# Performance work log

Measured on AMD Instinct MI355X. Metric: run time of the kernel, lower is better.

## Reference

```python
import jax, jax.numpy as jnp
import numpy as np

IN_F = 2048
OUT_F = 2048
BATCH = 8192
ACT_BITS = 4
EPS = 1e-5


def setup_inputs() -> dict:
    key = jax.random.key(0)
    kx, kw, kb = jax.random.split(key, 3)
    x = jax.random.normal(kx, (BATCH, IN_F), dtype=jnp.float32)
    # kaiming-uniform-like init: bound = sqrt(6/fan_in) with a=sqrt(5) -> gain sqrt(2/(1+5))
    bound_w = float(np.sqrt(6.0 / (1.0 + 5.0)) / np.sqrt(IN_F))
    weight = jax.random.uniform(kw, (OUT_F, IN_F), minval=-bound_w, maxval=bound_w, dtype=jnp.float32)
    bound_b = float(1.0 / np.sqrt(IN_F))
    bias = jax.random.uniform(kb, (OUT_F,), minval=-bound_b, maxval=bound_b, dtype=jnp.float32)
    return {"x": x, "weight": weight, "bias": bias}


def _ste_sign(x):
    return x + jax.lax.stop_gradient(jnp.sign(x) - x)


def _ste_clip(x, lo, hi):
    return x + jax.lax.stop_gradient(jnp.clip(x, lo, hi) - x)


def reference(x, weight, bias):
    # weight binarization (ternary-ish via sign of mean-centered rows)
    w_centered = weight - jnp.mean(weight, axis=1, keepdims=True)
    w_bin = _ste_sign(w_centered)                       # [out, in]
    beta = jnp.mean(jnp.abs(weight), axis=1)[None, :]   # [1, out]
    # layer norm (no affine) over last dim
    mu = jnp.mean(x, axis=-1, keepdims=True)
    var = jnp.mean((x - mu) ** 2, axis=-1, keepdims=True)
    xln = (x - mu) / jnp.sqrt(var + EPS)
    qb = float(2 ** (ACT_BITS - 1) - 1)
    gama = jnp.maximum(jnp.max(jnp.abs(xln), axis=-1, keepdims=True), EPS)  # [B,1]
    xq = _ste_clip(xln * (qb / gama), -qb + EPS, qb - EPS)
    y = jnp.einsum('bi,oi->bo', xq, w_bin)
    y = y * (beta * gama / qb)
    return y + bias
```

## Files before the change

### kernel.cpp

```cpp
#include <hip/hip_runtime.h>
#include <hip/hip_bf16.h>

#define BATCH 8192
#define IN_F  2048
#define OUT_F 2048
#define QB    7.0f
#define EPSV  1e-5f
#define ASCALE 18.0f

typedef char  i8x4 __attribute__((ext_vector_type(4)));
typedef int   i32x4 __attribute__((ext_vector_type(4)));

#define AS1(p) ((__attribute__((address_space(1))) void*)(p))
#define AS3(p) ((__attribute__((address_space(3))) void*)(p))

__device__ __forceinline__ float waveReduceSum(float v) {
#pragma unroll
  for (int off = 32; off > 0; off >>= 1) v += __shfl_xor(v, off, 64);
  return v;
}
__device__ __forceinline__ float waveReduceMax(float v) {
#pragma unroll
  for (int off = 32; off > 0; off >>= 1) v = fmaxf(v, __shfl_xor(v, off, 64));
  return v;
}

__global__ __launch_bounds__(256) void prep_kernel(const float* __restrict__ x,
                                                   const float* __restrict__ w,
                                                   char* __restrict__ xq,
                                                   char* __restrict__ wb,
                                                   float* __restrict__ gamaOut,
                                                   float* __restrict__ betaOut) {
  __shared__ float red[8];
  const int t = threadIdx.x;
  const int wave = t >> 6, lane = t & 63;

  if (blockIdx.x < OUT_F) {
    const int row = blockIdx.x;
    const float* wr = w + (size_t)row * IN_F;
    float4 v0 = ((const float4*)wr)[t];
    float4 v1 = ((const float4*)wr)[t + 256];
    float s  = v0.x + v0.y + v0.z + v0.w + v1.x + v1.y + v1.z + v1.w;
    float sa = fabsf(v0.x) + fabsf(v0.y) + fabsf(v0.z) + fabsf(v0.w)
             + fabsf(v1.x) + fabsf(v1.y) + fabsf(v1.z) + fabsf(v1.w);
    float wsum = waveReduceSum(s);
    float wsa  = waveReduceSum(sa);
    if (lane == 0) { red[wave] = wsum; red[4 + wave] = wsa; }
    __syncthreads();
    const float mu   = (red[0] + red[1] + red[2] + red[3]) * (1.0f / IN_F);
    const float beta = (red[4] + red[5] + red[6] + red[7]) * (1.0f / IN_F);
    if (t == 0) betaOut[row] = beta;

    char* wbr = wb + (size_t)row * IN_F;
    auto sgn = [&](float xv) -> char {
      float d = xv - mu;
      return (char)((d > 0.0f) ? 1 : (d < 0.0f ? -1 : 0));
    };
    i8x4 q0 = { sgn(v0.x), sgn(v0.y), sgn(v0.z), sgn(v0.w) };
    i8x4 q1 = { sgn(v1.x), sgn(v1.y), sgn(v1.z), sgn(v1.w) };
    ((i8x4*)wbr)[t]       = q0;
    ((i8x4*)wbr)[t + 256] = q1;
  } else {
    const int row = blockIdx.x - OUT_F;
    const float* xr = x + (size_t)row * IN_F;
    float4 v0 = ((const float4*)xr)[t];
    float4 v1 = ((const float4*)xr)[t + 256];
    float s  = v0.x + v0.y + v0.z + v0.w + v1.x + v1.y + v1.z + v1.w;
    float s2 = v0.x*v0.x + v0.y*v0.y + v0.z*v0.z + v0.w*v0.w
             + v1.x*v1.x + v1.y*v1.y + v1.z*v1.z + v1.w*v1.w;
    float wsum  = waveReduceSum(s);
    float wsum2 = waveReduceSum(s2);
    if (lane == 0) { red[wave] = wsum; red[4 + wave] = wsum2; }
    __syncthreads();
    const float mu  = (red[0] + red[1] + red[2] + red[3]) * (1.0f / IN_F);
    const float ex2 = (red[4] + red[5] + red[6] + red[7]) * (1.0f / IN_F);
    const float rstd = rsqrtf(fmaxf(ex2 - mu * mu, 0.0f) + EPSV);

    float n[8];
    n[0] = (v0.x - mu) * rstd; n[1] = (v0.y - mu) * rstd;
    n[2] = (v0.z - mu) * rstd; n[3] = (v0.w - mu) * rstd;
    n[4] = (v1.x - mu) * rstd; n[5] = (v1.y - mu) * rstd;
    n[6] = (v1.z - mu) * rstd; n[7] = (v1.w - mu) * rstd;
    float amax = 0.0f;
#pragma unroll
    for (int j = 0; j < 8; ++j) amax = fmaxf(amax, fabsf(n[j]));

    __syncthreads();
    float wmax = waveReduceMax(amax);
    if (lane == 0) red[wave] = wmax;
    __syncthreads();
    const float g = fmaxf(fmaxf(fmaxf(red[0], red[1]), fmaxf(red[2], red[3])), EPSV);
    if (t == 0) gamaOut[row] = g;

    const float qs = (QB * ASCALE) / g;
    const float lo = (-QB + EPSV) * ASCALE, hi = (QB - EPSV) * ASCALE;
    auto qz = [&](float v) -> char {
      return (char)__float2int_rn(fminf(fmaxf(v * qs, lo), hi));
    };
    char* xqr = xq + (size_t)row * IN_F;
    i8x4 q0 = { qz(n[0]), qz(n[1]), qz(n[2]), qz(n[3]) };
    i8x4 q1 = { qz(n[4]), qz(n[5]), qz(n[6]), qz(n[7]) };
    ((i8x4*)xqr)[t]       = q0;
    ((i8x4*)xqr)[t + 256] = q1;
  }
}

__global__ __launch_bounds__(256) void gemm_kernel(const char* __restrict__ A,
                                                   const char* __restrict__ B,
                                                   const float* __restrict__ beta,
                                                   const float* __restrict__ gama,
                                                   const float* __restrict__ bias,
                                                   float* __restrict__ out) {
  __shared__ __align__(16) char As[128 * 128];
  __shared__ __align__(16) char Bs[128 * 128];

  const int t = threadIdx.x;
  const int wave = t >> 6, lane = t & 63;
  const int mBase = blockIdx.y * 128;
  const int nBase = blockIdx.x * 128;
  const int wm = (wave >> 1) * 64;
  const int wn = (wave & 1) * 64;

  i32x4 acc[4][4];
#pragma unroll
  for (int i = 0; i < 4; ++i)
#pragma unroll
    for (int j = 0; j < 4; ++j) {
      i32x4 z = {0, 0, 0, 0};
      acc[i][j] = z;
    }

  const int lr = lane >> 3;
  const int ls = lane & 7;
  const int gch = (ls - lr) & 7;
  const char* aG[4];
  const char* bG[4];
  char* aL[4];
  char* bL[4];
#pragma unroll
  for (int j = 0; j < 4; ++j) {
    const int rowInTile = j * 32 + wave * 8 + lr;
    aG[j] = A + (size_t)(mBase + rowInTile) * IN_F + gch * 16;
    bG[j] = B + (size_t)(nBase + rowInTile) * IN_F + gch * 16;
    aL[j] = As + (j * 32 + wave * 8) * 128;
    bL[j] = Bs + (j * 32 + wave * 8) * 128;
  }

  const int fr = lane & 15;
  const int kq = lane >> 4;
  const char* aF = As + (wm + fr) * 128;
  const char* bF = Bs + (wn + fr) * 128;
  int koff[2];
#pragma unroll
  for (int ks = 0; ks < 2; ++ks) koff[ks] = ((ks * 4 + kq + fr) & 7) * 16;

  for (int k0 = 0; k0 < IN_F; k0 += 128) {
#pragma unroll
    for (int j = 0; j < 4; ++j) {
      __builtin_amdgcn_global_load_lds(AS1(aG[j] + k0), AS3(aL[j]), 16, 0, 0);
      __builtin_amdgcn_global_load_lds(AS1(bG[j] + k0), AS3(bL[j]), 16, 0, 0);
    }
    __syncthreads();

#pragma unroll
    for (int ks = 0; ks < 2; ++ks) {
      i32x4 af[4], bf[4];
#pragma unroll
      for (int mi = 0; mi < 4; ++mi) af[mi] = *(const i32x4*)(aF + mi * 16 * 128 + koff[ks]);
#pragma unroll
      for (int ni = 0; ni < 4; ++ni) bf[ni] = *(const i32x4*)(bF + ni * 16 * 128 + koff[ks]);
#pragma unroll
      for (int mi = 0; mi < 4; ++mi)
#pragma unroll
        for (int ni = 0; ni < 4; ++ni)
          acc[mi][ni] = __builtin_amdgcn_mfma_i32_16x16x64_i8(af[mi], bf[ni], acc[mi][ni], 0, 0, 0);
    }
    __syncthreads();
  }

  const float qinv = 1.0f / (QB * ASCALE);
  const int orow0 = mBase + wm + (kq << 2);
  const int ocol0 = nBase + wn + fr;
#pragma unroll
  for (int mi = 0; mi < 4; ++mi) {
    const int rbase = orow0 + mi * 16;
    const float g0 = gama[rbase + 0] * qinv;
    const float g1 = gama[rbase + 1] * qinv;
    const float g2 = gama[rbase + 2] * qinv;
    const float g3 = gama[rbase + 3] * qinv;
#pragma unroll
    for (int ni = 0; ni < 4; ++ni) {
      const int c = ocol0 + ni * 16;
      const float bsc = beta[c];
      const float bv  = bias[c];
      float* op = out + (size_t)rbase * OUT_F + c;
      op[0 * OUT_F] = (float)acc[mi][ni][0] * (bsc * g0) + bv;
      op[1 * OUT_F] = (float)acc[mi][ni][1] * (bsc * g1) + bv;
      op[2 * OUT_F] = (float)acc[mi][ni][2] * (bsc * g2) + bv;
      op[3 * OUT_F] = (float)acc[mi][ni][3] * (bsc * g3) + bv;
    }
  }
}

extern "C" void kernel_launch(void* const* d_in, const int* in_sizes, int n_in,
                              void* d_out, int out_size, void* d_ws, size_t ws_size,
                              hipStream_t stream) {
  const float* x      = (const float*)d_in[0];
  const float* weight = (const float*)d_in[1];
  const float* bias   = (const float*)d_in[2];
  float* out = (float*)d_out;

  char* ws = (char*)d_ws;
  char* wbin = ws;
  char* xq   = ws + (size_t)OUT_F * IN_F;
  float* betaW = (float*)(ws + (size_t)OUT_F * IN_F + (size_t)BATCH * IN_F);
  float* gamaX = betaW + OUT_F;

  prep_kernel<<<OUT_F + BATCH, 256, 0, stream>>>(x, weight, xq, wbin, gamaX, betaW);
  gemm_kernel<<<dim3(OUT_F / 128, BATCH / 128), 256, 0, stream>>>(xq, wbin, betaW, gamaX, bias, out);
}
```

Before: 170.2 us.

## Double-buffer int8 GEMM LDS tiles with K=64 stages to overlap loads

Splits the shared-memory A/B tiles into two 64-wide K buffers and prefetches the next K slice with global_load_lds while MFMAs run on the current one. This cuts the barriers per iteration from two to one and aims to hide global-to-LDS latency. The swizzle is adapted to 4 chunks per row. Risks: twice as many loop iterations with less MFMA work each, and possible reliance on the single barrier to order the async LDS loads.

```diff
diff --git a/kernel.cpp b/kernel.cpp
--- a/kernel.cpp
+++ b/kernel.cpp
@@ -111,8 +111,8 @@
                                                    const float* __restrict__ gama,
                                                    const float* __restrict__ bias,
                                                    float* __restrict__ out) {
-  __shared__ __align__(16) char As[128 * 128];
-  __shared__ __align__(16) char Bs[128 * 128];
+  __shared__ __align__(16) char As[2][128 * 64];
+  __shared__ __align__(16) char Bs[2][128 * 64];
 
   const int t = threadIdx.x;
   const int wave = t >> 6, lane = t & 63;
@@ -130,52 +130,60 @@
       acc[i][j] = z;
     }
 
-  const int lr = lane >> 3;
-  const int ls = lane & 7;
-  const int gch = (ls - lr) & 7;
-  const char* aG[4];
-  const char* bG[4];
-  char* aL[4];
-  char* bL[4];
-#pragma unroll
-  for (int j = 0; j < 4; ++j) {
-    const int rowInTile = j * 32 + wave * 8 + lr;
+  const int lr = lane >> 2;
+  const int ls = lane & 3;
+  const int gch = (ls - (lr >> 1)) & 3;
+  const char* aG[2];
+  const char* bG[2];
+  int ldsOff[2];
+#pragma unroll
+  for (int j = 0; j < 2; ++j) {
+    const int rowInTile = wave * 32 + j * 16 + lr;
     aG[j] = A + (size_t)(mBase + rowInTile) * IN_F + gch * 16;
     bG[j] = B + (size_t)(nBase + rowInTile) * IN_F + gch * 16;
-    aL[j] = As + (j * 32 + wave * 8) * 128;
-    bL[j] = Bs + (j * 32 + wave * 8) * 128;
+    ldsOff[j] = (wave * 32 + j * 16) * 64;
   }
 
   const int fr = lane & 15;
   const int kq = lane >> 4;
-  const char* aF = As + (wm + fr) * 128;
-  const char* bF = Bs + (wn + fr) * 128;
-  int koff[2];
-#pragma unroll
-  for (int ks = 0; ks < 2; ++ks) koff[ks] = ((ks * 4 + kq + fr) & 7) * 16;
-
-  for (int k0 = 0; k0 < IN_F; k0 += 128) {
-#pragma unroll
-    for (int j = 0; j < 4; ++j) {
-      __builtin_amdgcn_global_load_lds(AS1(aG[j] + k0), AS3(aL[j]), 16, 0, 0);
-      __builtin_amdgcn_global_load_lds(AS1(bG[j] + k0), AS3(bL[j]), 16, 0, 0);
+  const int koff = ((kq + (fr >> 1)) & 3) * 16;
+  const int aFoff = (wm + fr) * 64 + koff;
+  const int bFoff = (wn + fr) * 64 + koff;
+
+#pragma unroll
+  for (int j = 0; j < 2; ++j) {
+    __builtin_amdgcn_global_load_lds(AS1(aG[j]), AS3(&As[0][0] + ldsOff[j]), 16, 0, 0);
+    __builtin_amdgcn_global_load_lds(AS1(bG[j]), AS3(&Bs[0][0] + ldsOff[j]), 16, 0, 0);
+  }
+
+  int cur = 0;
+  for (int it = 0; it < IN_F / 64; ++it) {
+    __syncthreads();
+    if (it + 1 < IN_F / 64) {
+      const int k0 = (it + 1) * 64;
+      char* aDst = &As[cur ^ 1][0];
+      char* bDst = &Bs[cur ^ 1][0];
+#pragma unroll
+      for (int j = 0; j < 2; ++j) {
+        __builtin_amdgcn_global_load_lds(AS1(aG[j] + k0), AS3(aDst + ldsOff[j]), 16, 0, 0);
+        __builtin_amdgcn_global_load_lds(AS1(bG[j] + k0), AS3(bDst + ldsOff[j]), 16, 0, 0);
+      }
     }
-    __syncthreads();
-
-#pragma unroll
-    for (int ks = 0; ks < 2; ++ks) {
-      i32x4 af[4], bf[4];
-#pragma unroll
-      for (int mi = 0; mi < 4; ++mi) af[mi] = *(const i32x4*)(aF + mi * 16 * 128 + koff[ks]);
-#pragma unroll
-      for (int ni = 0; ni < 4; ++ni) bf[ni] = *(const i32x4*)(bF + ni * 16 * 128 + koff[ks]);
-#pragma unroll
-      for (int mi = 0; mi < 4; ++mi)
-#pragma unroll
-        for (int ni = 0; ni < 4; ++ni)
-          acc[mi][ni] = __builtin_amdgcn_mfma_i32_16x16x64_i8(af[mi], bf[ni], acc[mi][ni], 0, 0, 0);
-    }
-    __syncthreads();
+
+    const char* aF = &As[cur][0] + aFoff;
+    const char* bF = &Bs[cur][0] + bFoff;
+    i32x4 af[4], bf[4];
+#pragma unroll
+    for (int mi = 0; mi < 4; ++mi) af[mi] = *(const i32x4*)(aF + mi * 16 * 64);
+#pragma unroll
+    for (int ni = 0; ni < 4; ++ni) bf[ni] = *(const i32x4*)(bF + ni * 16 * 64);
+#pragma unroll
+    for (int mi = 0; mi < 4; ++mi)
+#pragma unroll
+      for (int ni = 0; ni < 4; ++ni)
+        acc[mi][ni] = __builtin_amdgcn_mfma_i32_16x16x64_i8(af[mi], bf[ni], acc[mi][ni], 0, 0, 0);
+
+    cur ^= 1;
   }
 
   const float qinv = 1.0f / (QB * ASCALE);
```

After: 174.1 us. 1.02x slower.
